# Kernel tuning notes

Measured on AMD Instinct MI355X. Metric: run time of the kernel, lower is better.

The kernel has to match this reference:

```python
import jax, jax.numpy as jnp
import numpy as np

N_NODES = 50000
N_EDGES = 800000
IN_FEATS = 128
N_HIDDEN = 64
OUT_FEATS = 40
DIM = 8  # pseudo-coordinate dimension
K = 1    # n_kernels


def setup_inputs() -> dict:
    key = jax.random.key(0)
    ks = jax.random.split(key, 12)
    inp = {
        "features": jax.random.normal(ks[0], (N_NODES, IN_FEATS), dtype=jnp.float32),
        "edge_weight": jax.random.normal(ks[1], (N_EDGES, DIM), dtype=jnp.float32),
        "src": jax.random.randint(ks[2], (N_EDGES,), 0, N_NODES),
        "dst": jax.random.randint(ks[3], (N_EDGES,), 0, N_NODES),
        # layer 1 params (fc has no bias in DGL GMMConv; separate additive bias)
        "W1": jax.random.normal(ks[4], (IN_FEATS, K * N_HIDDEN), dtype=jnp.float32) * (1.0 / np.sqrt(IN_FEATS)),
        "b1": jnp.zeros((N_HIDDEN,), dtype=jnp.float32),
        "mu1": jax.random.normal(ks[5], (K, DIM), dtype=jnp.float32) * 0.1,
        "inv_sigma1": jnp.ones((K, DIM), dtype=jnp.float32),
        # layer 2 params
        "W2": jax.random.normal(ks[6], (N_HIDDEN, K * OUT_FEATS), dtype=jnp.float32) * (1.0 / np.sqrt(N_HIDDEN)),
        "b2": jnp.zeros((OUT_FEATS,), dtype=jnp.float32),
        "mu2": jax.random.normal(ks[7], (K, DIM), dtype=jnp.float32) * 0.1,
        "inv_sigma2": jnp.ones((K, DIM), dtype=jnp.float32),
    }
    return inp


def gmm_conv(x, pseudo, src, dst, W, b, mu, inv_sigma, out_feats):
    # x: [N, in], pseudo: [E, DIM], W: [in, K*out]
    h = (x @ W).reshape(-1, K, out_feats)                      # [N, K, out]
    # gaussian mixture weights per edge/kernel: [E, K]
    diff = pseudo[:, None, :] - mu[None, :, :]                 # [E, K, DIM]
    gw = jnp.exp(-0.5 * jnp.sum(diff * diff * (inv_sigma[None] ** 2), axis=-1))
    # gather src feats, weight, sum over kernels: [E, out]
    msg = jnp.einsum("ekf,ek->ef", h[src], gw)
    agg = jax.ops.segment_sum(msg, dst, num_segments=N_NODES)  # [N, out]
    return agg + b


def reference(features, edge_weight, src, dst, W1, b1, mu1, inv_sigma1, W2, b2, mu2, inv_sigma2):
    x = gmm_conv(features, edge_weight, src, dst, W1, b1, mu1, inv_sigma1, N_HIDDEN)
    x = gmm_conv(x, edge_weight, src, dst, W2, b2, mu2, inv_sigma2, OUT_FEATS)
    return jax.nn.log_softmax(x, axis=1)
```

## Files before the change

kernel.cpp:

```cpp
#include <hip/hip_runtime.h>
#include <hip/hip_fp16.h>
#include <math.h>

#define N_NODES 50000
#define N_EDGES 800000
#define IN_FEATS 128
#define N_HIDDEN 64
#define OUT_FEATS 40
#define DIM 8
#define GT_TILES ((N_NODES + 63) / 64)
#define FILL_BLOCKS (N_EDGES / 256)
#define SCAN_NB ((N_NODES + 255) / 256)

typedef _Float16 half8 __attribute__((ext_vector_type(8)));
typedef float floatx4 __attribute__((ext_vector_type(4)));

__device__ __forceinline__ int wave_incl_scan(int x, int lane) {
#pragma unroll
    for (int off = 1; off < 64; off <<= 1) {
        int v = __shfl_up(x, off, 64);
        if (lane >= off) x += v;
    }
    return x;
}

__global__ __launch_bounds__(256) void hist_kernel(const int* __restrict__ dst,
                                                   int* __restrict__ counts,
                                                   unsigned short* __restrict__ rank) {
    int i = blockIdx.x * 256 + threadIdx.x;
    if (i * 4 >= N_EDGES) return;
    int4 d = ((const int4*)dst)[i];
    ushort4 r;
    r.x = (unsigned short)atomicAdd(&counts[d.x], 1);
    r.y = (unsigned short)atomicAdd(&counts[d.y], 1);
    r.z = (unsigned short)atomicAdd(&counts[d.z], 1);
    r.w = (unsigned short)atomicAdd(&counts[d.w], 1);
    ((ushort4*)rank)[i] = r;
}

__global__ __launch_bounds__(256) void scan_partial_kernel(const int* __restrict__ counts,
                                                           int* __restrict__ offsets,
                                                           int* __restrict__ partials) {
    const int tid = threadIdx.x, bid = blockIdx.x;
    const int i = bid * 256 + tid;
    const int lane = tid & 63, wid = tid >> 6;
    int x = (i < N_NODES) ? counts[i] : 0;
    int incl = wave_incl_scan(x, lane);
    __shared__ int wsum[4];
    if (lane == 63) wsum[wid] = incl;
    __syncthreads();
    int base = 0;
#pragma unroll
    for (int w = 0; w < 4; ++w)
        if (w < wid) base += wsum[w];
    if (i < N_NODES) offsets[i] = base + incl - x;
    if (tid == 255) partials[bid] = base + incl;
}

__global__ __launch_bounds__(256) void scan_base_kernel(int* __restrict__ partials) {
    const int tid = threadIdx.x;
    const int lane = tid & 63, wid = tid >> 6;
    int x = (tid < SCAN_NB) ? partials[tid] : 0;
    int incl = wave_incl_scan(x, lane);
    __shared__ int wsum[4];
    if (lane == 63) wsum[wid] = incl;
    __syncthreads();
    int base = 0;
#pragma unroll
    for (int w = 0; w < 4; ++w)
        if (w < wid) base += wsum[w];
    if (tid < SCAN_NB) partials[tid] = base + incl - x;
}

__global__ __launch_bounds__(256) void scan_add_kernel(int* __restrict__ offsets,
                                                       const int* __restrict__ partials) {
    const int i = blockIdx.x * 256 + threadIdx.x;
    if (i < N_NODES) offsets[i] += partials[blockIdx.x];
    if (i == N_NODES) offsets[N_NODES] = N_EDGES;
}

__global__ __launch_bounds__(256) void fillgemm_kernel(
    const float* __restrict__ features, const float* __restrict__ W1,
    const int* __restrict__ src, const int* __restrict__ dst,
    const float* __restrict__ ew,
    const float* __restrict__ mu1, const float* __restrict__ is1,
    const float* __restrict__ mu2, const float* __restrict__ is2,
    const int* __restrict__ offsets, const unsigned short* __restrict__ rank,
    int2* __restrict__ csr, __half* __restrict__ h1)
{
    const int tid = threadIdx.x;
    __shared__ __align__(16) __half WT[64][136];

    if (blockIdx.x >= GT_TILES) {
        int e = (blockIdx.x - GT_TILES) * 256 + tid;
        int sN = src[e];
        int dN = dst[e];
        unsigned short rk = rank[e];
        const float4* ew4 = (const float4*)(ew + (size_t)e * DIM);
        float4 wa = ew4[0], wb = ew4[1];
        float v[8] = {wa.x, wa.y, wa.z, wa.w, wb.x, wb.y, wb.z, wb.w};
        float s1 = 0.f, s2 = 0.f;
#pragma unroll
        for (int d = 0; d < DIM; ++d) {
            float d1 = v[d] - mu1[d]; float a1 = is1[d];
            float d2 = v[d] - mu2[d]; float a2 = is2[d];
            s1 += d1 * d1 * a1 * a1;
            s2 += d2 * d2 * a2 * a2;
        }
        __half2 g = __floats2half2_rn(expf(-0.5f * s1), expf(-0.5f * s2));
        int2 rec;
        rec.x = sN;
        rec.y = *reinterpret_cast<int*>(&g);
        int pos = offsets[dN] + rk;
        __builtin_nontemporal_store(*reinterpret_cast<long long*>(&rec),
                                    reinterpret_cast<long long*>(&csr[pos]));
        return;
    }

    int nodeBase = blockIdx.x * 64;
    for (int rep = 0; rep < 32; ++rep) {
        int idx = tid + rep * 256;
        int k = idx >> 6, n = idx & 63;
        WT[n][k] = __float2half(W1[idx]);
    }
    __syncthreads();

    int lane = tid & 63, w = tid >> 6;
    int m = lane & 15, quad = lane >> 4;
    int row = nodeBase + w * 16 + m;
    int rowc = (row < N_NODES) ? row : (N_NODES - 1);
    const float* fr = features + (size_t)rowc * IN_FEATS;

    floatx4 acc0 = {0.f,0.f,0.f,0.f}, acc1 = acc0, acc2 = acc0, acc3 = acc0;
#pragma unroll
    for (int kc = 0; kc < 4; ++kc) {
        float4 fa = *(const float4*)(fr + kc * 32 + quad * 8);
        float4 fb = *(const float4*)(fr + kc * 32 + quad * 8 + 4);
        union { half8 v; __half2 h2[4]; } A;
        A.h2[0] = __floats2half2_rn(fa.x, fa.y);
        A.h2[1] = __floats2half2_rn(fa.z, fa.w);
        A.h2[2] = __floats2half2_rn(fb.x, fb.y);
        A.h2[3] = __floats2half2_rn(fb.z, fb.w);
        half8 b0 = *(const half8*)&WT[ 0 + m][kc * 32 + quad * 8];
        half8 b1 = *(const half8*)&WT[16 + m][kc * 32 + quad * 8];
        half8 b2 = *(const half8*)&WT[32 + m][kc * 32 + quad * 8];
        half8 b3 = *(const half8*)&WT[48 + m][kc * 32 + quad * 8];
        acc0 = __builtin_amdgcn_mfma_f32_16x16x32_f16(A.v, b0, acc0, 0, 0, 0);
        acc1 = __builtin_amdgcn_mfma_f32_16x16x32_f16(A.v, b1, acc1, 0, 0, 0);
        acc2 = __builtin_amdgcn_mfma_f32_16x16x32_f16(A.v, b2, acc2, 0, 0, 0);
        acc3 = __builtin_amdgcn_mfma_f32_16x16x32_f16(A.v, b3, acc3, 0, 0, 0);
    }
    int nodeRow = nodeBase + w * 16 + quad * 4;
#pragma unroll
    for (int r = 0; r < 4; ++r) {
        int n = nodeRow + r;
        if (n < N_NODES) {
            size_t base = (size_t)n * N_HIDDEN + m;
            h1[base +  0] = __float2half(acc0[r]);
            h1[base + 16] = __float2half(acc1[r]);
            h1[base + 32] = __float2half(acc2[r]);
            h1[base + 48] = __float2half(acc3[r]);
        }
    }
}

__global__ __launch_bounds__(256) void agg1_gemm2_kernel(const __half* __restrict__ h,
                                                         const int* __restrict__ offsets,
                                                         const int2* __restrict__ csr,
                                                         const float* __restrict__ b,
                                                         const float* __restrict__ W2,
                                                         __half* __restrict__ h2) {
    __shared__ float xs[8][64];
    const unsigned* h32 = (const unsigned*)h;
    const int tid = threadIdx.x;
    const int w = tid >> 6, lane = tid & 63;
    const int hf = lane >> 5, p = lane & 31;
    const int ln = w * 2 + hf;
    const int n = blockIdx.x * 8 + ln;
    int beg = offsets[n], end = offsets[n + 1];

    float ax = 0.f, ay = 0.f;
    int j = beg;
    for (; j + 4 <= end; j += 4) {
        int2 r0 = csr[j + 0], r1 = csr[j + 1], r2 = csr[j + 2], r3 = csr[j + 3];
        unsigned v0 = h32[(size_t)r0.x * 32 + p];
        unsigned v1 = h32[(size_t)r1.x * 32 + p];
        unsigned v2 = h32[(size_t)r2.x * 32 + p];
        unsigned v3 = h32[(size_t)r3.x * 32 + p];
        float g0 = __low2float(*reinterpret_cast<__half2*>(&r0.y));
        float g1 = __low2float(*reinterpret_cast<__half2*>(&r1.y));
        float g2 = __low2float(*reinterpret_cast<__half2*>(&r2.y));
        float g3 = __low2float(*reinterpret_cast<__half2*>(&r3.y));
        float2 f0 = __half22float2(*reinterpret_cast<__half2*>(&v0));
        float2 f1 = __half22float2(*reinterpret_cast<__half2*>(&v1));
        float2 f2 = __half22float2(*reinterpret_cast<__half2*>(&v2));
        float2 f3 = __half22float2(*reinterpret_cast<__half2*>(&v3));
        ax += f0.x * g0; ay += f0.y * g0;
        ax += f1.x * g1; ay += f1.y * g1;
        ax += f2.x * g2; ay += f2.y * g2;
        ax += f3.x * g3; ay += f3.y * g3;
    }
    for (; j < end; ++j) {
        int2 r = csr[j];
        unsigned v = h32[(size_t)r.x * 32 + p];
        float g = __low2float(*reinterpret_cast<__half2*>(&r.y));
        float2 f = __half22float2(*reinterpret_cast<__half2*>(&v));
        ax += f.x * g; ay += f.y * g;
    }
    float2 bb = *(const float2*)&b[2 * p];
    *(float2*)&xs[ln][2 * p] = make_float2(ax + bb.x, ay + bb.y);
    __syncthreads();

    for (int o = tid; o < 8 * OUT_FEATS; o += 256) {
        int node = o / OUT_FEATS, t = o % OUT_FEATS;
        const float* xr = xs[node];
        float acc = 0.f;
#pragma unroll
        for (int k = 0; k < N_HIDDEN; ++k)
            acc += xr[k] * W2[k * OUT_FEATS + t];
        h2[(size_t)(blockIdx.x * 8 + node) * OUT_FEATS + t] = __float2half(acc);
    }
}

__global__ __launch_bounds__(256) void agg2_kernel(const __half* __restrict__ h,
                                                   const int* __restrict__ offsets,
                                                   const int2* __restrict__ csr,
                                                   const float* __restrict__ b,
                                                   float* __restrict__ out) {
    const unsigned* h32 = (const unsigned*)h;
    const int tid = threadIdx.x;
    const int w = tid >> 6, lane = tid & 63;
    const int hf = lane >> 5, p = lane & 31;
    const int n = blockIdx.x * 8 + w * 2 + hf;
    const int pc = (p < 20) ? p : 19;
    int beg = offsets[n], end = offsets[n + 1];

    float ax = 0.f, ay = 0.f;
    int j = beg;
    for (; j + 4 <= end; j += 4) {
        int2 r0 = csr[j + 0], r1 = csr[j + 1], r2 = csr[j + 2], r3 = csr[j + 3];
        unsigned v0 = h32[(size_t)r0.x * 20 + pc];
        unsigned v1 = h32[(size_t)r1.x * 20 + pc];
        unsigned v2 = h32[(size_t)r2.x * 20 + pc];
        unsigned v3 = h32[(size_t)r3.x * 20 + pc];
        float g0 = __high2float(*reinterpret_cast<__half2*>(&r0.y));
        float g1 = __high2float(*reinterpret_cast<__half2*>(&r1.y));
        float g2 = __high2float(*reinterpret_cast<__half2*>(&r2.y));
        float g3 = __high2float(*reinterpret_cast<__half2*>(&r3.y));
        float2 f0 = __half22float2(*reinterpret_cast<__half2*>(&v0));
        float2 f1 = __half22float2(*reinterpret_cast<__half2*>(&v1));
        float2 f2 = __half22float2(*reinterpret_cast<__half2*>(&v2));
        float2 f3 = __half22float2(*reinterpret_cast<__half2*>(&v3));
        ax += f0.x * g0; ay += f0.y * g0;
        ax += f1.x * g1; ay += f1.y * g1;
        ax += f2.x * g2; ay += f2.y * g2;
        ax += f3.x * g3; ay += f3.y * g3;
    }
    for (; j < end; ++j) {
        int2 r = csr[j];
        unsigned v = h32[(size_t)r.x * 20 + pc];
        float g = __high2float(*reinterpret_cast<__half2*>(&r.y));
        float2 f = __half22float2(*reinterpret_cast<__half2*>(&v));
        ax += f.x * g; ay += f.y * g;
    }

    bool valid = (p < 20);
    float vx = valid ? ax + b[2 * p]     : -INFINITY;
    float vy = valid ? ay + b[2 * p + 1] : -INFINITY;
    float m = fmaxf(vx, vy);
#pragma unroll
    for (int off = 16; off; off >>= 1)
        m = fmaxf(m, __shfl_xor(m, off, 32));
    float ex = valid ? (expf(vx - m) + expf(vy - m)) : 0.f;
#pragma unroll
    for (int off = 16; off; off >>= 1)
        ex += __shfl_xor(ex, off, 32);
    float ls = logf(ex);
    if (valid) {
        float2 o = make_float2(vx - m - ls, vy - m - ls);
        *(float2*)&out[(size_t)n * OUT_FEATS + 2 * p] = o;
    }
}

extern "C" void kernel_launch(void* const* d_in, const int* in_sizes, int n_in,
                              void* d_out, int out_size, void* d_ws, size_t ws_size,
                              hipStream_t stream) {
    const float* features    = (const float*)d_in[0];
    const float* edge_weight = (const float*)d_in[1];
    const int*   src         = (const int*)d_in[2];
    const int*   dst         = (const int*)d_in[3];
    const float* W1          = (const float*)d_in[4];
    const float* b1          = (const float*)d_in[5];
    const float* mu1         = (const float*)d_in[6];
    const float* is1         = (const float*)d_in[7];
    const float* W2          = (const float*)d_in[8];
    const float* b2          = (const float*)d_in[9];
    const float* mu2         = (const float*)d_in[10];
    const float* is2         = (const float*)d_in[11];
    float* out = (float*)d_out;

    int2*           csr     = (int2*)d_ws;
    __half*         h1      = (__half*)(csr + N_EDGES);
    __half*         h2      = h1 + (size_t)N_NODES * N_HIDDEN;
    int*            counts  = (int*)(h2 + (size_t)N_NODES * OUT_FEATS);
    unsigned short* rank    = (unsigned short*)(counts + N_NODES);
    int*            offsets = (int*)(rank + N_EDGES);
    int*            partials= offsets + N_NODES + 1;

    hipMemsetAsync(counts, 0, N_NODES * sizeof(int), stream);

    hist_kernel<<<(N_EDGES / 4 + 255) / 256, 256, 0, stream>>>(dst, counts, rank);

    scan_partial_kernel<<<SCAN_NB, 256, 0, stream>>>(counts, offsets, partials);
    scan_base_kernel<<<1, 256, 0, stream>>>(partials);
    scan_add_kernel<<<SCAN_NB, 256, 0, stream>>>(offsets, partials);

    fillgemm_kernel<<<GT_TILES + FILL_BLOCKS, 256, 0, stream>>>(
        features, W1, src, dst, edge_weight, mu1, is1, mu2, is2, offsets, rank, csr, h1);

    agg1_gemm2_kernel<<<N_NODES / 8, 256, 0, stream>>>(h1, offsets, csr, b1, W2, h2);

    agg2_kernel<<<N_NODES / 8, 256, 0, stream>>>(h2, offsets, csr, b2, out);
}
```

Baseline: 236.4 us.

## Use one wave per node with 8-byte gathers in agg1 and stage W2 in LDS

The layer-1 aggregation now gives each node a full wave instead of a half wave. Four 16-lane groups each gather 8-byte chunks from different edges, and their partial sums are combined with xor shuffles. This is meant to keep more edge loads in flight per node. W2 (10 KB) is copied into shared memory in every block, so the small GEMM reads from LDS instead of global memory. The cost is twice as many blocks, with each one repeating the W2 copy, and padded lanes are wasted when the edge count is low (average degree is about 16).

```diff
diff --git a/kernel.cpp b/kernel.cpp
--- a/kernel.cpp
+++ b/kernel.cpp
@@ -170,55 +170,62 @@
                                                          const float* __restrict__ b,
                                                          const float* __restrict__ W2,
                                                          __half* __restrict__ h2) {
-    __shared__ float xs[8][64];
-    const unsigned* h32 = (const unsigned*)h;
+    __shared__ float xs[4][64];
+    __shared__ float W2s[N_HIDDEN * OUT_FEATS];
+    const uint2* h64 = (const uint2*)h;
     const int tid = threadIdx.x;
     const int w = tid >> 6, lane = tid & 63;
-    const int hf = lane >> 5, p = lane & 31;
-    const int ln = w * 2 + hf;
-    const int n = blockIdx.x * 8 + ln;
+    const int g = lane >> 4, p = lane & 15;
+    const int n = blockIdx.x * 4 + w;
+
+    for (int i = tid; i < N_HIDDEN * OUT_FEATS; i += 256)
+        W2s[i] = W2[i];
+
     int beg = offsets[n], end = offsets[n + 1];
 
-    float ax = 0.f, ay = 0.f;
-    int j = beg;
-    for (; j + 4 <= end; j += 4) {
-        int2 r0 = csr[j + 0], r1 = csr[j + 1], r2 = csr[j + 2], r3 = csr[j + 3];
-        unsigned v0 = h32[(size_t)r0.x * 32 + p];
-        unsigned v1 = h32[(size_t)r1.x * 32 + p];
-        unsigned v2 = h32[(size_t)r2.x * 32 + p];
-        unsigned v3 = h32[(size_t)r3.x * 32 + p];
-        float g0 = __low2float(*reinterpret_cast<__half2*>(&r0.y));
-        float g1 = __low2float(*reinterpret_cast<__half2*>(&r1.y));
-        float g2 = __low2float(*reinterpret_cast<__half2*>(&r2.y));
-        float g3 = __low2float(*reinterpret_cast<__half2*>(&r3.y));
-        float2 f0 = __half22float2(*reinterpret_cast<__half2*>(&v0));
-        float2 f1 = __half22float2(*reinterpret_cast<__half2*>(&v1));
-        float2 f2 = __half22float2(*reinterpret_cast<__half2*>(&v2));
-        float2 f3 = __half22float2(*reinterpret_cast<__half2*>(&v3));
-        ax += f0.x * g0; ay += f0.y * g0;
-        ax += f1.x * g1; ay += f1.y * g1;
-        ax += f2.x * g2; ay += f2.y * g2;
-        ax += f3.x * g3; ay += f3.y * g3;
-    }
-    for (; j < end; ++j) {
-        int2 r = csr[j];
-        unsigned v = h32[(size_t)r.x * 32 + p];
-        float g = __low2float(*reinterpret_cast<__half2*>(&r.y));
-        float2 f = __half22float2(*reinterpret_cast<__half2*>(&v));
-        ax += f.x * g; ay += f.y * g;
-    }
-    float2 bb = *(const float2*)&b[2 * p];
-    *(float2*)&xs[ln][2 * p] = make_float2(ax + bb.x, ay + bb.y);
+    float ax0 = 0.f, ax1 = 0.f, ax2 = 0.f, ax3 = 0.f;
+    for (int j = beg; j < end; j += 8) {
+        int ja = j + g, jb = j + g + 4;
+        int2 ra = csr[(ja < end) ? ja : (end - 1)];
+        int2 rb = csr[(jb < end) ? jb : (end - 1)];
+        float ga = (ja < end) ? __low2float(*reinterpret_cast<__half2*>(&ra.y)) : 0.f;
+        float gb = (jb < end) ? __low2float(*reinterpret_cast<__half2*>(&rb.y)) : 0.f;
+        uint2 va = h64[(size_t)ra.x * 16 + p];
+        uint2 vb = h64[(size_t)rb.x * 16 + p];
+        float2 a0 = __half22float2(*reinterpret_cast<__half2*>(&va.x));
+        float2 a1 = __half22float2(*reinterpret_cast<__half2*>(&va.y));
+        float2 b0 = __half22float2(*reinterpret_cast<__half2*>(&vb.x));
+        float2 b1 = __half22float2(*reinterpret_cast<__half2*>(&vb.y));
+        ax0 += a0.x * ga; ax1 += a0.y * ga;
+        ax2 += a1.x * ga; ax3 += a1.y * ga;
+        ax0 += b0.x * gb; ax1 += b0.y * gb;
+        ax2 += b1.x * gb; ax3 += b1.y * gb;
+    }
+    ax0 += __shfl_xor(ax0, 16, 64); ax1 += __shfl_xor(ax1, 16, 64);
+    ax2 += __shfl_xor(ax2, 16, 64); ax3 += __shfl_xor(ax3, 16, 64);
+    ax0 += __shfl_xor(ax0, 32, 64); ax1 += __shfl_xor(ax1, 32, 64);
+    ax2 += __shfl_xor(ax2, 32, 64); ax3 += __shfl_xor(ax3, 32, 64);
+
+    if (g == 0) {
+        float4 bb = *(const float4*)&b[4 * p];
+        *(float4*)&xs[w][4 * p] =
+            make_float4(ax0 + bb.x, ax1 + bb.y, ax2 + bb.z, ax3 + bb.w);
+    }
     __syncthreads();
 
-    for (int o = tid; o < 8 * OUT_FEATS; o += 256) {
-        int node = o / OUT_FEATS, t = o % OUT_FEATS;
+    if (tid < 4 * OUT_FEATS) {
+        int node = tid / OUT_FEATS, t = tid % OUT_FEATS;
         const float* xr = xs[node];
         float acc = 0.f;
 #pragma unroll
-        for (int k = 0; k < N_HIDDEN; ++k)
-            acc += xr[k] * W2[k * OUT_FEATS + t];
-        h2[(size_t)(blockIdx.x * 8 + node) * OUT_FEATS + t] = __float2half(acc);
+        for (int k = 0; k < N_HIDDEN; k += 4) {
+            float4 x4 = *(const float4*)&xr[k];
+            acc += x4.x * W2s[(k + 0) * OUT_FEATS + t];
+            acc += x4.y * W2s[(k + 1) * OUT_FEATS + t];
+            acc += x4.z * W2s[(k + 2) * OUT_FEATS + t];
+            acc += x4.w * W2s[(k + 3) * OUT_FEATS + t];
+        }
+        h2[(size_t)(blockIdx.x * 4 + node) * OUT_FEATS + t] = __float2half(acc);
     }
 }
 
@@ -318,7 +325,7 @@
     fillgemm_kernel<<<GT_TILES + FILL_BLOCKS, 256, 0, stream>>>(
         features, W1, src, dst, edge_weight, mu1, is1, mu2, is2, offsets, rank, csr, h1);
 
-    agg1_gemm2_kernel<<<N_NODES / 8, 256, 0, stream>>>(h1, offsets, csr, b1, W2, h2);
+    agg1_gemm2_kernel<<<N_NODES / 4, 256, 0, stream>>>(h1, offsets, csr, b1, W2, h2);
 
     agg2_kernel<<<N_NODES / 8, 256, 0, stream>>>(h2, offsets, csr, b2, out);
 }
```

Result: slower. 244.3 us (+3.3%).
